# Performance work log

Measured on AMD Instinct MI355X. Metric: run time of the kernel, lower is better.

## Reference

```python
import jax, jax.numpy as jnp
import numpy as np

# Module config (matches init_kwargs)
B, H, W, C = 2, 64, 64, 128
NH, K = 4, 7            # num_heads, kernel_size (odd)
HD = C // NH            # head_dim = 32
SCALE = HD ** -0.5


def setup_inputs() -> dict:
    key = jax.random.key(0)
    ks = jax.random.split(key, 5)
    return {
        "x": jax.random.normal(ks[0], (B, H, W, C), jnp.float32),
        "w_qkv": jax.random.normal(ks[1], (C, 3 * C), jnp.float32) * 0.02,
        "b_qkv": jnp.zeros((3 * C,), jnp.float32),
        "rpb": jax.random.normal(ks[2], (NH, 2 * K - 1, 2 * K - 1), jnp.float32) * 0.02,
        "w_proj": jax.random.normal(ks[3], (C, C), jnp.float32) * 0.02,
        "b_proj": jnp.zeros((C,), jnp.float32),
    }


def _window_starts(L):
    # NATTEN clamped window start: max(i-k//2,0), shifted left at right border so the
    # full k-window fits. clip handles both cases since i-k//2 > L-k  <=>  i+k//2 >= L.
    i = jnp.arange(L)
    return jnp.clip(i - K // 2, 0, L - K)  # [L]


def reference(x, w_qkv, b_qkv, rpb, w_proj, b_proj):
    # qkv projection: [B,H,W,3,NH,HD]
    qkv = (x @ w_qkv + b_qkv).reshape(B, H, W, 3, NH, HD)
    q = qkv[..., 0, :, :] * SCALE  # [B,H,W,NH,HD]
    k = qkv[..., 1, :, :]
    v = qkv[..., 2, :, :]

    a = jnp.arange(K)
    idx_h = _window_starts(H)[:, None] + a[None, :]  # [H,K] key rows per query row
    idx_w = _window_starts(W)[:, None] + a[None, :]  # [W,K] key cols per query col

    # Gather k*k neighborhoods (honors the local sparsity; no [HW,HW] matrix):
    # k[:, idx_h] -> [B,H,K,W,NH,HD]; then index W axis -> [B,H,K,W,K,NH,HD]
    k_nb = k[:, idx_h][:, :, :, idx_w]
    v_nb = v[:, idx_h][:, :, :, idx_w]

    # natten2dqkrpb: attn[b,n,i,j,p,q] = <q[b,i,j,n], k[b, ih[i,p], iw[j,q], n]>
    attn = jnp.einsum('bhwnd,bhpwqnd->bnhwpq', q, k_nb)  # [B,NH,H,W,K,K]

    # relative position bias index = (neighbor - query) + (k-1) per axis
    bidx_h = idx_h - jnp.arange(H)[:, None] + (K - 1)  # [H,K] in [0, 2k-2]
    bidx_w = idx_w - jnp.arange(W)[:, None] + (K - 1)  # [W,K]
    bias = rpb[:, bidx_h[:, :, None, None], bidx_w[None, None]]  # [NH,H,K,W,K]
    attn = attn + bias.transpose(0, 1, 3, 2, 4)[None]  # -> [1,NH,H,W,K,K]

    # softmax over the flattened k*k neighborhood
    attn = jax.nn.softmax(attn.reshape(B, NH, H, W, K * K), axis=-1)
    attn = attn.reshape(B, NH, H, W, K, K)

    # natten2dav: weighted sum over neighborhood values
    out = jnp.einsum('bnhwpq,bhpwqnd->bhwnd', attn, v_nb).reshape(B, H, W, C)
    return out @ w_proj + b_proj
```

## Files before the change

kernel.cpp:

```cpp
#include <hip/hip_runtime.h>
#include <hip/hip_bf16.h>
#include <cstddef>

#define BB 2
#define HH 64
#define WW 64
#define SCALE 0.17677669529663687f

#define HALO_H 10
#define HALO_W 14
#define NPIX 140
#define NQ 32

typedef short short8 __attribute__((ext_vector_type(8)));
typedef float f32x4 __attribute__((ext_vector_type(4)));

#if defined(__has_builtin)
#if __has_builtin(__builtin_amdgcn_fdot2_f32_bf16)
#define HAS_BFDOT2 1
#endif
#endif
#ifndef HAS_BFDOT2
#define HAS_BFDOT2 0
#endif

#if HAS_BFDOT2
typedef __bf16 v2bf __attribute__((ext_vector_type(2)));
__device__ inline float bfdot2(uint a, uint b, float c) {
    union { uint u; v2bf v; } ua, ub;
    ua.u = a; ub.u = b;
    return __builtin_amdgcn_fdot2_f32_bf16(ua.v, ub.v, c, false);
}
#endif

__device__ inline ushort f2bf(float f) {
    union { __hip_bfloat16 b; ushort u; } cv;
    cv.b = __float2bfloat16(f);
    return cv.u;
}
__device__ inline float bflo(uint u) { union { uint i; float f; } c; c.i = u << 16; return c.f; }
__device__ inline float bfhi(uint u) { union { uint i; float f; } c; c.i = u & 0xffff0000u; return c.f; }

__global__ __launch_bounds__(256) void qkv_gemm_fused_kernel(
    const float* __restrict__ x, const float* __restrict__ w_qkv,
    const float* __restrict__ b_qkv, const float* __restrict__ w_proj,
    ushort* __restrict__ qkv, ushort* __restrict__ Wp_t)
{
    __shared__ ushort S[64 * 128 + 96 * 128];
    ushort* As = S;
    ushort* Bs = S + 64 * 128;

    const int tid = threadIdx.x;
    const int m0 = blockIdx.x * 64;
    const int n0 = blockIdx.y * 96;

    if (blockIdx.y == 0 && tid < 128)
        Wp_t[(size_t)blockIdx.x * 128 + tid] =
            f2bf(w_proj[(size_t)tid * 128 + blockIdx.x]);

    #pragma unroll
    for (int t = 0; t < 4; ++t) {
        int idx = tid + t * 256;
        int r = idx >> 4, c = idx & 15;
        const float* src = x + (size_t)(m0 + r) * 128 + c * 8;
        float4 v0 = *(const float4*)src;
        float4 v1 = *(const float4*)(src + 4);
        union { ushort s[8]; uint4 q; } u;
        u.s[0] = f2bf(v0.x); u.s[1] = f2bf(v0.y); u.s[2] = f2bf(v0.z); u.s[3] = f2bf(v0.w);
        u.s[4] = f2bf(v1.x); u.s[5] = f2bf(v1.y); u.s[6] = f2bf(v1.z); u.s[7] = f2bf(v1.w);
        *(uint4*)&As[r * 128 + (c ^ (r & 7)) * 8] = u.q;
    }
    #pragma unroll
    for (int t = 0; t < 6; ++t) {
        int idx = tid + t * 256;
        int kc = idx / 96, n = idx - kc * 96;
        union { ushort s[8]; uint4 q; } u;
        #pragma unroll
        for (int e = 0; e < 8; ++e)
            u.s[e] = f2bf(w_qkv[(size_t)(kc * 8 + e) * 384 + n0 + n]);
        *(uint4*)&Bs[n * 128 + ((kc ^ (n & 7)) * 8)] = u.q;
    }
    __syncthreads();

    const int wid = tid >> 6, lane = tid & 63;
    const int l15 = lane & 15, l4 = lane >> 4;
    const int mr = (wid >> 1) * 32, nr = (wid & 1) * 48;

    f32x4 acc[2][3] = {};
    #pragma unroll
    for (int ks = 0; ks < 4; ++ks) {
        short8 af[2], bf[3];
        #pragma unroll
        for (int fm = 0; fm < 2; ++fm) {
            int row = mr + fm * 16 + l15;
            af[fm] = *(const short8*)&As[row * 128 + ((ks * 4 + l4) ^ (row & 7)) * 8];
        }
        #pragma unroll
        for (int fn = 0; fn < 3; ++fn) {
            int row = nr + fn * 16 + l15;
            bf[fn] = *(const short8*)&Bs[row * 128 + ((ks * 4 + l4) ^ (row & 7)) * 8];
        }
        #pragma unroll
        for (int fm = 0; fm < 2; ++fm)
            #pragma unroll
            for (int fn = 0; fn < 3; ++fn)
                acc[fm][fn] = __builtin_amdgcn_mfma_f32_16x16x32_bf16(
                    af[fm], bf[fn], acc[fm][fn], 0, 0, 0);
    }

    __syncthreads();
    ushort* C_s = S;
    #pragma unroll
    for (int fn = 0; fn < 3; ++fn) {
        int colb = nr + fn * 16;
        int col = colb + l15;
        float bc = b_qkv[n0 + col];
        float sc = (n0 + colb < 128) ? SCALE : 1.0f;
        #pragma unroll
        for (int fm = 0; fm < 2; ++fm)
            #pragma unroll
            for (int reg = 0; reg < 4; ++reg) {
                int row = mr + fm * 16 + l4 * 4 + reg;
                C_s[row * 200 + col] = f2bf((acc[fm][fn][reg] + bc) * sc);
            }
    }
    __syncthreads();
    #pragma unroll
    for (int t = 0; t < 3; ++t) {
        int idx = tid + t * 256;
        int row = idx / 12, c = idx - row * 12;
        uint4 v = *(const uint4*)&C_s[row * 200 + c * 8];
        *(uint4*)&qkv[(size_t)(m0 + row) * 384 + n0 + c * 8] = v;
    }
}

__global__ __launch_bounds__(256) void natten_proj_kernel(
    const ushort* __restrict__ qkv,
    const float* __restrict__ rpb,
    const ushort* __restrict__ Wp_t,
    const float* __restrict__ b_proj,
    float* __restrict__ out)
{
    __shared__ ushort KV_s[4][NPIX * 64];
    __shared__ ushort AO_s[NQ * 128];
    __shared__ float rpb_s[676];

    const int tid = threadIdx.x;
    const int wv = tid >> 6;
    const int lane = tid & 63;
    const int bx = ((blockIdx.x & 7) << 5) | (blockIdx.x >> 3);
    const int b  = bx >> 7;
    const int th = (bx >> 3) & 15;
    const int tw = bx & 7;
    const int h0 = th * 4, w0 = tw * 8;
    const int ho = max(0, h0 - 3), wo = max(0, w0 - 3);

    #pragma unroll
    for (int t = 0; t < 3; ++t) {
        int idx = tid + t * 256;
        if (idx < 676) rpb_s[idx] = rpb[idx];
    }

    ushort* KV = &KV_s[wv][0];
    #pragma unroll
    for (int t = 0; t < 18; ++t) {
        int idx = lane + t * 64;
        if (idx < NPIX * 8) {
            int pix = idx >> 3, s = idx & 7;
            int r = pix / HALO_W, c = pix - r * HALO_W;
            int gh = min(ho + r, HH - 1), gw = min(wo + c, WW - 1);
            const ushort* gp = qkv + (size_t)((b << 12) + (gh << 6) + gw) * 384
                               + 128 + (s >> 2) * 128 + wv * 32 + (s & 3) * 8;
            uint4 v = *(const uint4*)gp;
            int bb = (pix >> 2) & 1;
            int slot = (2 * ((s & 3) ^ (pix & 3)) ^ bb) ^ (s >> 2);
            *(uint4*)&KV[pix * 64 + slot * 8] = v;
        }
    }

    const int q = lane >> 1, half = lane & 1;
    const int qh = h0 + (q >> 3), qw = w0 + (q & 7);
    const int hs = min(max(qh - 3, 0), HH - 7);
    const int ws = min(max(qw - 3, 0), WW - 7);
    const int base_lp = (hs - ho) * HALO_W + (ws - wo);
    const int bh0 = hs - qh + 6, bw0 = ws - qw + 6;
    const size_t qpix = (size_t)((b << 12) + (qh << 6) + qw);

#if HAS_BFDOT2
    uint4 qb[4];
    #pragma unroll
    for (int d4 = 0; d4 < 4; ++d4)
        qb[d4] = *(const uint4*)(qkv + qpix * 384 + wv * 32 + d4 * 8);
#else
    float qf[32];
    #pragma unroll
    for (int d4 = 0; d4 < 4; ++d4) {
        uint4 qu = *(const uint4*)(qkv + qpix * 384 + wv * 32 + d4 * 8);
        qf[d4*8+0] = bflo(qu.x); qf[d4*8+1] = bfhi(qu.x);
        qf[d4*8+2] = bflo(qu.y); qf[d4*8+3] = bfhi(qu.y);
        qf[d4*8+4] = bflo(qu.z); qf[d4*8+5] = bfhi(qu.z);
        qf[d4*8+6] = bflo(qu.w); qf[d4*8+7] = bfhi(qu.w);
    }
#endif
    __syncthreads();

    float lg[25];
    #pragma unroll
    for (int i = 0; i < 25; ++i) {
        int j = half + 2 * i;
        float s = -1e30f;
        if (j < 49) {
            int p = (j * 37) >> 8;
            int qq = j - p * 7;
            int lp = base_lp + p * HALO_W + qq;
            int bb = (lp >> 2) & 1;
            float a = 0.f;
            #pragma unroll
            for (int d4 = 0; d4 < 4; ++d4) {
                uint4 ku = *(const uint4*)&KV[lp * 64 + ((2 * (d4 ^ (lp & 3)) ^ bb) * 8)];
#if HAS_BFDOT2
                a = bfdot2(ku.x, qb[d4].x, a);
                a = bfdot2(ku.y, qb[d4].y, a);
                a = bfdot2(ku.z, qb[d4].z, a);
                a = bfdot2(ku.w, qb[d4].w, a);
#else
                a += bflo(ku.x)*qf[d4*8+0] + bfhi(ku.x)*qf[d4*8+1]
                   + bflo(ku.y)*qf[d4*8+2] + bfhi(ku.y)*qf[d4*8+3]
                   + bflo(ku.z)*qf[d4*8+4] + bfhi(ku.z)*qf[d4*8+5]
                   + bflo(ku.w)*qf[d4*8+6] + bfhi(ku.w)*qf[d4*8+7];
#endif
            }
            s = a + rpb_s[wv * 169 + (bh0 + p) * 13 + (bw0 + qq)];
        }
        lg[i] = s;
    }

    float m = lg[0];
    #pragma unroll
    for (int i = 1; i < 25; ++i) m = fmaxf(m, lg[i]);
    m = fmaxf(m, __shfl_xor(m, 1));
    float ssum = 0.f;
    #pragma unroll
    for (int i = 0; i < 25; ++i) {
        int j = half + 2 * i;
        lg[i] = (j < 49) ? __expf(lg[i] - m) : 0.f;
        ssum += lg[i];
    }
    ssum += __shfl_xor(ssum, 1);
    float inv = 1.f / ssum;
    #pragma unroll
    for (int i = 0; i < 25; ++i) lg[i] *= inv;

    float o[32] = {};
    #pragma unroll
    for (int i = 0; i < 25; ++i) {
        int j = half + 2 * i;
        if (j < 49) {
            int p = (j * 37) >> 8;
            int qq = j - p * 7;
            int lp = base_lp + p * HALO_W + qq;
            int bb = (lp >> 2) & 1;
            float a = lg[i];
            #pragma unroll
            for (int d4 = 0; d4 < 4; ++d4) {
                uint4 vu = *(const uint4*)&KV[lp * 64 + (((2 * (d4 ^ (lp & 3)) ^ bb) ^ 1) * 8)];
                o[d4*8+0] += a * bflo(vu.x); o[d4*8+1] += a * bfhi(vu.x);
                o[d4*8+2] += a * bflo(vu.y); o[d4*8+3] += a * bfhi(vu.y);
                o[d4*8+4] += a * bflo(vu.z); o[d4*8+5] += a * bfhi(vu.z);
                o[d4*8+6] += a * bflo(vu.w); o[d4*8+7] += a * bfhi(vu.w);
            }
        }
    }
    #pragma unroll
    for (int e = 0; e < 32; ++e) o[e] += __shfl_xor(o[e], 1);

    #pragma unroll
    for (int cc = 0; cc < 2; ++cc) {
        int d4 = half * 2 + cc;
        union { ushort s[8]; uint4 u4; } w;
        #pragma unroll
        for (int e = 0; e < 8; ++e) w.s[e] = f2bf(o[d4 * 8 + e]);
        *(uint4*)&AO_s[q * 128 + (((wv * 4 + d4) ^ (q & 7)) * 8)] = w.u4;
    }
    __syncthreads();

    const int l15 = lane & 15, l4 = lane >> 4;
    const int wr = wv >> 1, wc = wv & 1;

    f32x4 pacc[4] = {};
    #pragma unroll
    for (int ks = 0; ks < 4; ++ks) {
        int arow = wr * 16 + l15;
        short8 af = *(const short8*)&AO_s[arow * 128 + ((ks * 4 + l4) ^ (arow & 7)) * 8];
        #pragma unroll
        for (int fn = 0; fn < 4; ++fn) {
            int brow = wc * 64 + fn * 16 + l15;
            short8 bf = *(const short8*)(Wp_t + (size_t)brow * 128 + (ks * 4 + l4) * 8);
            pacc[fn] = __builtin_amdgcn_mfma_f32_16x16x32_bf16(af, bf, pacc[fn], 0, 0, 0);
        }
    }
    #pragma unroll
    for (int fn = 0; fn < 4; ++fn) {
        int col = wc * 64 + fn * 16 + l15;
        float bc = b_proj[col];
        #pragma unroll
        for (int reg = 0; reg < 4; ++reg) {
            int q2 = wr * 16 + l4 * 4 + reg;
            int oh = h0 + (q2 >> 3), ow = w0 + (q2 & 7);
            out[(size_t)((b << 12) + (oh << 6) + ow) * 128 + col] = pacc[fn][reg] + bc;
        }
    }
}

extern "C" void kernel_launch(void* const* d_in, const int* in_sizes, int n_in,
                              void* d_out, int out_size, void* d_ws, size_t ws_size,
                              hipStream_t stream)
{
    const float* x      = (const float*)d_in[0];
    const float* w_qkv  = (const float*)d_in[1];
    const float* b_qkv  = (const float*)d_in[2];
    const float* rpb    = (const float*)d_in[3];
    const float* w_proj = (const float*)d_in[4];
    const float* b_proj = (const float*)d_in[5];
    float* out = (float*)d_out;

    const int M = BB * HH * WW;
    ushort* qkv  = (ushort*)d_ws;
    ushort* Wp_t = qkv + (size_t)M * 384;

    qkv_gemm_fused_kernel<<<dim3(128, 4), 256, 0, stream>>>(
        x, w_qkv, b_qkv, w_proj, qkv, Wp_t);

    natten_proj_kernel<<<256, 256, 0, stream>>>(
        qkv, rpb, Wp_t, b_proj, out);
}
```

Measured before the change: 30.34 us.

## Split each query's neighborhood across four lanes with 512-thread natten blocks

Doubles the natten_proj block to 512 threads: two waves share each head's K/V halo, and each query's 49 neighbors are split across four lanes instead of two. The softmax max/sum and output accumulators gain an extra shuffle-reduction stage, and the projection GEMM is re-tiled so each of the eight waves computes 32 output columns. The aim is more parallelism and latency hiding in the attention phase, since only 256 blocks exist. The cost is more cross-lane shuffles and fewer blocks co-resident per CU.

```diff
diff --git a/kernel.cpp b/kernel.cpp
--- a/kernel.cpp
+++ b/kernel.cpp
@@ -134,7 +134,7 @@
     }
 }
 
-__global__ __launch_bounds__(256) void natten_proj_kernel(
+__global__ __launch_bounds__(512, 2) void natten_proj_kernel(
     const ushort* __restrict__ qkv,
     const float* __restrict__ rpb,
     const ushort* __restrict__ Wp_t,
@@ -147,6 +147,8 @@
 
     const int tid = threadIdx.x;
     const int wv = tid >> 6;
+    const int hd = wv >> 1;
+    const int sub = wv & 1;
     const int lane = tid & 63;
     const int bx = ((blockIdx.x & 7) << 5) | (blockIdx.x >> 3);
     const int b  = bx >> 7;
@@ -156,29 +158,33 @@
     const int ho = max(0, h0 - 3), wo = max(0, w0 - 3);
 
     #pragma unroll
-    for (int t = 0; t < 3; ++t) {
-        int idx = tid + t * 256;
+    for (int t = 0; t < 2; ++t) {
+        int idx = tid + t * 512;
         if (idx < 676) rpb_s[idx] = rpb[idx];
     }
 
-    ushort* KV = &KV_s[wv][0];
-    #pragma unroll
-    for (int t = 0; t < 18; ++t) {
-        int idx = lane + t * 64;
-        if (idx < NPIX * 8) {
-            int pix = idx >> 3, s = idx & 7;
-            int r = pix / HALO_W, c = pix - r * HALO_W;
-            int gh = min(ho + r, HH - 1), gw = min(wo + c, WW - 1);
-            const ushort* gp = qkv + (size_t)((b << 12) + (gh << 6) + gw) * 384
-                               + 128 + (s >> 2) * 128 + wv * 32 + (s & 3) * 8;
-            uint4 v = *(const uint4*)gp;
-            int bb = (pix >> 2) & 1;
-            int slot = (2 * ((s & 3) ^ (pix & 3)) ^ bb) ^ (s >> 2);
-            *(uint4*)&KV[pix * 64 + slot * 8] = v;
-        }
-    }
-
-    const int q = lane >> 1, half = lane & 1;
+    ushort* KV = &KV_s[hd][0];
+    {
+        const int sidx = sub * 64 + lane;
+        #pragma unroll
+        for (int t = 0; t < 9; ++t) {
+            int idx = sidx + t * 128;
+            if (idx < NPIX * 8) {
+                int pix = idx >> 3, s = idx & 7;
+                int r = pix / HALO_W, c = pix - r * HALO_W;
+                int gh = min(ho + r, HH - 1), gw = min(wo + c, WW - 1);
+                const ushort* gp = qkv + (size_t)((b << 12) + (gh << 6) + gw) * 384
+                                   + 128 + (s >> 2) * 128 + hd * 32 + (s & 3) * 8;
+                uint4 v = *(const uint4*)gp;
+                int bb = (pix >> 2) & 1;
+                int slot = (2 * ((s & 3) ^ (pix & 3)) ^ bb) ^ (s >> 2);
+                *(uint4*)&KV[pix * 64 + slot * 8] = v;
+            }
+        }
+    }
+
+    const int q = sub * 16 + (lane >> 2);
+    const int t4 = lane & 3;
     const int qh = h0 + (q >> 3), qw = w0 + (q & 7);
     const int hs = min(max(qh - 3, 0), HH - 7);
     const int ws = min(max(qw - 3, 0), WW - 7);
@@ -190,12 +196,12 @@
     uint4 qb[4];
     #pragma unroll
     for (int d4 = 0; d4 < 4; ++d4)
-        qb[d4] = *(const uint4*)(qkv + qpix * 384 + wv * 32 + d4 * 8);
+        qb[d4] = *(const uint4*)(qkv + qpix * 384 + hd * 32 + d4 * 8);
 #else
     float qf[32];
     #pragma unroll
     for (int d4 = 0; d4 < 4; ++d4) {
-        uint4 qu = *(const uint4*)(qkv + qpix * 384 + wv * 32 + d4 * 8);
+        uint4 qu = *(const uint4*)(qkv + qpix * 384 + hd * 32 + d4 * 8);
         qf[d4*8+0] = bflo(qu.x); qf[d4*8+1] = bfhi(qu.x);
         qf[d4*8+2] = bflo(qu.y); qf[d4*8+3] = bfhi(qu.y);
         qf[d4*8+4] = bflo(qu.z); qf[d4*8+5] = bfhi(qu.z);
@@ -204,10 +210,10 @@
 #endif
     __syncthreads();
 
-    float lg[25];
-    #pragma unroll
-    for (int i = 0; i < 25; ++i) {
-        int j = half + 2 * i;
+    float lg[13];
+    #pragma unroll
+    for (int i = 0; i < 13; ++i) {
+        int j = t4 + 4 * i;
         float s = -1e30f;
         if (j < 49) {
             int p = (j * 37) >> 8;
@@ -230,31 +236,33 @@
                    + bflo(ku.w)*qf[d4*8+6] + bfhi(ku.w)*qf[d4*8+7];
 #endif
             }
-            s = a + rpb_s[wv * 169 + (bh0 + p) * 13 + (bw0 + qq)];
+            s = a + rpb_s[hd * 169 + (bh0 + p) * 13 + (bw0 + qq)];
         }
         lg[i] = s;
     }
 
     float m = lg[0];
     #pragma unroll
-    for (int i = 1; i < 25; ++i) m = fmaxf(m, lg[i]);
+    for (int i = 1; i < 13; ++i) m = fmaxf(m, lg[i]);
     m = fmaxf(m, __shfl_xor(m, 1));
+    m = fmaxf(m, __shfl_xor(m, 2));
     float ssum = 0.f;
     #pragma unroll
-    for (int i = 0; i < 25; ++i) {
-        int j = half + 2 * i;
+    for (int i = 0; i < 13; ++i) {
+        int j = t4 + 4 * i;
         lg[i] = (j < 49) ? __expf(lg[i] - m) : 0.f;
         ssum += lg[i];
     }
     ssum += __shfl_xor(ssum, 1);
+    ssum += __shfl_xor(ssum, 2);
     float inv = 1.f / ssum;
     #pragma unroll
-    for (int i = 0; i < 25; ++i) lg[i] *= inv;
+    for (int i = 0; i < 13; ++i) lg[i] *= inv;
 
     float o[32] = {};
     #pragma unroll
-    for (int i = 0; i < 25; ++i) {
-        int j = half + 2 * i;
+    for (int i = 0; i < 13; ++i) {
+        int j = t4 + 4 * i;
         if (j < 49) {
             int p = (j * 37) >> 8;
             int qq = j - p * 7;
@@ -273,39 +281,50 @@
     }
     #pragma unroll
     for (int e = 0; e < 32; ++e) o[e] += __shfl_xor(o[e], 1);
-
-    #pragma unroll
-    for (int cc = 0; cc < 2; ++cc) {
-        int d4 = half * 2 + cc;
-        union { ushort s[8]; uint4 u4; } w;
-        #pragma unroll
-        for (int e = 0; e < 8; ++e) w.s[e] = f2bf(o[d4 * 8 + e]);
-        *(uint4*)&AO_s[q * 128 + (((wv * 4 + d4) ^ (q & 7)) * 8)] = w.u4;
+    float t16v[16];
+    const int dbase = (lane & 1) * 16;
+    #pragma unroll
+    for (int e = 0; e < 16; ++e) {
+        float v = o[dbase + e];
+        v += __shfl_xor(v, 2);
+        t16v[e] = v;
+    }
+
+    if ((lane & 2) == 0) {
+        #pragma unroll
+        for (int cc = 0; cc < 2; ++cc) {
+            int d4 = (lane & 1) * 2 + cc;
+            union { ushort s[8]; uint4 u4; } w;
+            #pragma unroll
+            for (int e = 0; e < 8; ++e) w.s[e] = f2bf(t16v[cc * 8 + e]);
+            *(uint4*)&AO_s[q * 128 + (((hd * 4 + d4) ^ (q & 7)) * 8)] = w.u4;
+        }
     }
     __syncthreads();
 
     const int l15 = lane & 15, l4 = lane >> 4;
-    const int wr = wv >> 1, wc = wv & 1;
-
-    f32x4 pacc[4] = {};
+    const int wr2 = wv >> 2;
+    const int wc4 = wv & 3;
+
+    f32x4 pacc[2] = {};
     #pragma unroll
     for (int ks = 0; ks < 4; ++ks) {
-        int arow = wr * 16 + l15;
+        int arow = wr2 * 16 + l15;
         short8 af = *(const short8*)&AO_s[arow * 128 + ((ks * 4 + l4) ^ (arow & 7)) * 8];
         #pragma unroll
-        for (int fn = 0; fn < 4; ++fn) {
-            int brow = wc * 64 + fn * 16 + l15;
+        for (int fn = 0; fn < 2; ++fn) {
+            int brow = wc4 * 32 + fn * 16 + l15;
             short8 bf = *(const short8*)(Wp_t + (size_t)brow * 128 + (ks * 4 + l4) * 8);
             pacc[fn] = __builtin_amdgcn_mfma_f32_16x16x32_bf16(af, bf, pacc[fn], 0, 0, 0);
         }
     }
     #pragma unroll
-    for (int fn = 0; fn < 4; ++fn) {
-        int col = wc * 64 + fn * 16 + l15;
+    for (int fn = 0; fn < 2; ++fn) {
+        int col = wc4 * 32 + fn * 16 + l15;
         float bc = b_proj[col];
         #pragma unroll
         for (int reg = 0; reg < 4; ++reg) {
-            int q2 = wr * 16 + l4 * 4 + reg;
+            int q2 = wr2 * 16 + l4 * 4 + reg;
             int oh = h0 + (q2 >> 3), ow = w0 + (q2 & 7);
             out[(size_t)((b << 12) + (oh << 6) + ow) * 128 + col] = pacc[fn][reg] + bc;
         }
@@ -331,6 +350,6 @@
     qkv_gemm_fused_kernel<<<dim3(128, 4), 256, 0, stream>>>(
         x, w_qkv, b_qkv, w_proj, qkv, Wp_t);
 
-    natten_proj_kernel<<<256, 256, 0, stream>>>(
+    natten_proj_kernel<<<256, 512, 0, stream>>>(
         qkv, rpb, Wp_t, b_proj, out);
 }
```

Result: slower. 49.08 us (+61.8%).
